# Performance work log

Hardware: AMD Instinct MI355X
Metric: run time of the kernel (lower is better)

The kernel has to match this reference:

```python
import jax, jax.numpy as jnp
import numpy as np

NUM_RBF = 16
TOP_K = 30
NUM_POS_EMB = 16
EDGE_FEATURES = 128
MAX_REL_POS = 32  # ProteinMPNN max_relative_feature


def _rbf(D):
    # D: [...,]; returns [..., NUM_RBF]
    D_min, D_max = 2.0, 22.0
    D_mu = jnp.linspace(D_min, D_max, NUM_RBF)
    D_sigma = (D_max - D_min) / NUM_RBF
    return jnp.exp(-((D[..., None] - D_mu) / D_sigma) ** 2)


def _dist(Xca, mask, eps=1e-6):
    # Xca: [B,L,3], mask: [B,L]
    mask_2D = mask[:, :, None] * mask[:, None, :]  # [B,L,L]
    dX = Xca[:, :, None, :] - Xca[:, None, :, :]
    D = mask_2D * jnp.sqrt(jnp.sum(dX * dX, -1) + eps)
    D_max = jnp.max(D, -1, keepdims=True)
    D_adjust = D + (1.0 - mask_2D) * D_max
    L = Xca.shape[1]
    k = min(TOP_K, L)
    neg_topk, E_idx = jax.lax.top_k(-D_adjust, k)  # smallest distances
    return -neg_topk, E_idx  # D_neighbors:[B,L,K], E_idx:[B,L,K] int32


def _gather_nodes_pair(A, E_idx):
    # A: [B,L], E_idx: [B,L,K] -> [B,L,K]
    return jnp.take_along_axis(A[:, None, :].repeat(A.shape[1], 1), E_idx, axis=2)


def _rbf_pair(A, B_, E_idx):
    # A,B_: [B,L,3]; distances from A[i] to B_[j] for j in neighbors of i
    Bn = jnp.take_along_axis(B_[:, None, :, :].repeat(B_.shape[1], 1), E_idx[..., None].repeat(3, -1), axis=2)  # [B,L,K,3]
    D = jnp.sqrt(jnp.sum((A[:, :, None, :] - Bn) ** 2, -1) + 1e-6)
    return _rbf(D)


def setup_inputs() -> dict:
    key = jax.random.key(0)
    k1, k2, k3, k4 = jax.random.split(key, 4)
    B, L = 8, 2048
    X = jax.random.normal(k1, (B, L, 4, 3), dtype=jnp.float32) * 5.0
    mask = jnp.ones((B, L), dtype=jnp.float32)
    residue_idx = jnp.broadcast_to(jnp.arange(L, dtype=jnp.int32), (B, L))
    chain_labels = jnp.zeros((B, L), dtype=jnp.int32)
    in_dim = NUM_POS_EMB + NUM_RBF * 25  # 16 + 400 = 416
    W_e = jax.random.normal(k2, (in_dim, EDGE_FEATURES), dtype=jnp.float32) * (1.0 / np.sqrt(in_dim))
    b_e = jnp.zeros((EDGE_FEATURES,), dtype=jnp.float32)
    g_e = jnp.ones((EDGE_FEATURES,), dtype=jnp.float32)  # layernorm gamma
    be_ln = jnp.zeros((EDGE_FEATURES,), dtype=jnp.float32)  # layernorm beta
    pe_dim = 2 * MAX_REL_POS + 2  # 66
    W_pe = jax.random.normal(k3, (pe_dim, NUM_POS_EMB), dtype=jnp.float32) * (1.0 / np.sqrt(pe_dim))
    b_pe = jnp.zeros((NUM_POS_EMB,), dtype=jnp.float32)
    return {"X": X, "mask": mask, "residue_idx": residue_idx, "chain_labels": chain_labels,
            "W_e": W_e, "b_e": b_e, "g_e": g_e, "be_ln": be_ln, "W_pe": W_pe, "b_pe": b_pe}


def reference(X, mask, residue_idx, chain_labels, W_e, b_e, g_e, be_ln, W_pe, b_pe):
    # atoms
    N = X[:, :, 0, :]
    Ca = X[:, :, 1, :]
    C = X[:, :, 2, :]
    O = X[:, :, 3, :]
    # virtual Cb (ProteinMPNN formula)
    b = Ca - N
    c = C - Ca
    a = jnp.cross(b, c)
    Cb = -0.58273431 * a + 0.56802827 * b - 0.54067466 * c + Ca

    D_neighbors, E_idx = _dist(Ca, mask)

    atoms = {"N": N, "Ca": Ca, "C": C, "O": O, "Cb": Cb}
    order = ["Ca", "N", "C", "O", "Cb"]
    rbf_list = []
    for ai in order:
        for aj in order:
            if ai == "Ca" and aj == "Ca":
                rbf_list.append(_rbf(D_neighbors))
            else:
                rbf_list.append(_rbf_pair(atoms[ai], atoms[aj], E_idx))
    RBF_all = jnp.concatenate(rbf_list, axis=-1)  # [B,L,K,400]

    # positional encodings (ProteinMPNN style)
    offset = residue_idx[:, :, None] - residue_idx[:, None, :]  # [B,L,L]
    offset = jnp.take_along_axis(offset, E_idx, axis=2)  # [B,L,K]
    d_chains = (chain_labels[:, :, None] == chain_labels[:, None, :]).astype(jnp.int32)
    E_chains = jnp.take_along_axis(d_chains, E_idx, axis=2)  # [B,L,K]
    d = jnp.clip(offset + MAX_REL_POS, 0, 2 * MAX_REL_POS) * E_chains + (1 - E_chains) * (2 * MAX_REL_POS + 1)
    d_onehot = jax.nn.one_hot(d, 2 * MAX_REL_POS + 2, dtype=RBF_all.dtype)
    E_pos = d_onehot @ W_pe + b_pe  # [B,L,K,16]

    E = jnp.concatenate([E_pos, RBF_all], axis=-1)  # [B,L,K,416]
    E = E @ W_e + b_e  # [B,L,K,128]
    # layer norm
    mu = jnp.mean(E, -1, keepdims=True)
    var = jnp.var(E, -1, keepdims=True)
    E = (E - mu) / jnp.sqrt(var + 1e-5) * g_e + be_ln
    return E, E_idx
```

## Files before the change

kernel.cpp:

```cpp
#include <hip/hip_runtime.h>
#include <hip/hip_bf16.h>
#include <stdint.h>

#define BB   8
#define LL   2048
#define KK   30
#define COUT 128
#define FIN  416
#define PE_DIM 16
#define MAXREL 32
#define KSTEPS 13

typedef __attribute__((ext_vector_type(8))) short short8;
typedef __attribute__((ext_vector_type(4))) float f32x4;

__device__ __forceinline__ unsigned int f2bf(float x) {
    unsigned int u = __float_as_uint(x);
    return (u + 0x7fffu + ((u >> 16) & 1u)) >> 16;
}

__device__ __forceinline__ unsigned int packbf2(float a, float b) {
    float2 f; f.x = a; f.y = b;
    __hip_bfloat162 h = __float22bfloat162_rn(f);
    unsigned int u;
    __builtin_memcpy(&u, &h, 4);
    return u;
}

__device__ __forceinline__ short8 as_s8(uint4 u) {
    union { uint4 u; short8 s; } x; x.u = u; return x.s;
}

__device__ __forceinline__ int lanes_below(unsigned long long m) {
    return __builtin_amdgcn_mbcnt_hi((unsigned)(m >> 32),
           __builtin_amdgcn_mbcnt_lo((unsigned)m, 0));
}

__global__ __launch_bounds__(256)
void atoms_kernel(const float* __restrict__ X, float4* __restrict__ atoms4) {
    int idx = blockIdx.x * 256 + threadIdx.x;
    if (idx >= BB * LL) return;
    int b = idx >> 11;
    int i = idx & (LL - 1);
    const float4* xp = reinterpret_cast<const float4*>(X + (size_t)idx * 12);
    float4 p0 = xp[0], p1 = xp[1], p2 = xp[2];
    float Nx = p0.x, Ny = p0.y, Nz = p0.z;
    float Ax = p0.w, Ay = p1.x, Az = p1.y;
    float Cx = p1.z, Cy = p1.w, Cz = p2.x;
    float Ox = p2.y, Oy = p2.z, Oz = p2.w;
    float bx = Ax - Nx, by = Ay - Ny, bz = Az - Nz;
    float cx = Cx - Ax, cy = Cy - Ay, cz = Cz - Az;
    float ax = by * cz - bz * cy;
    float ay = bz * cx - bx * cz;
    float az = bx * cy - by * cx;
    float Cbx = -0.58273431f * ax + 0.56802827f * bx - 0.54067466f * cx + Ax;
    float Cby = -0.58273431f * ay + 0.56802827f * by - 0.54067466f * cy + Ay;
    float Cbz = -0.58273431f * az + 0.56802827f * bz - 0.54067466f * cz + Az;
    float4* ab = atoms4 + (size_t)b * 5 * LL;
    ab[0 * LL + i] = make_float4(Ax, Ay, Az, 0.f);
    ab[1 * LL + i] = make_float4(Nx, Ny, Nz, 0.f);
    ab[2 * LL + i] = make_float4(Cx, Cy, Cz, 0.f);
    ab[3 * LL + i] = make_float4(Ox, Oy, Oz, 0.f);
    ab[4 * LL + i] = make_float4(Cbx, Cby, Cbz, 0.f);
}

__global__ __launch_bounds__(256)
void wfrag_kernel(const float* __restrict__ W_e, unsigned short* __restrict__ wf) {
    int idx = blockIdx.x * 256 + threadIdx.x;
    if (idx >= KSTEPS * 8 * 64) return;
    int lane = idx & 63;
    int tile = idx >> 6;
    int ks = tile >> 3, nt = tile & 7;
    int n  = nt * 16 + (lane & 15);
    int kb = ks * 32 + (lane >> 4) * 8;
    unsigned int p[8];
    #pragma unroll
    for (int j = 0; j < 8; j++) p[j] = f2bf(W_e[(size_t)(kb + j) * COUT + n]);
    uint4 w;
    w.x = p[0] | (p[1] << 16);
    w.y = p[2] | (p[3] << 16);
    w.z = p[4] | (p[5] << 16);
    w.w = p[6] | (p[7] << 16);
    reinterpret_cast<uint4*>(wf)[idx] = w;
}

__global__ __launch_bounds__(256)
void topk_kernel(const float4* __restrict__ atoms4, unsigned short* __restrict__ eidx,
                 float* __restrict__ out_eidx_f) {
    __shared__ unsigned long long skeys[4][32];
    int t = threadIdx.x;
    int wv = t >> 6, ln = t & 63;
    int row = blockIdx.x * 4 + wv;
    int b = row >> 11, i = row & (LL - 1);
    const float4* cab = atoms4 + (size_t)b * 5 * LL;
    float4 pi = cab[i];
    float xi = pi.x, yi = pi.y, zi = pi.z;
    unsigned int bits[32];
    unsigned int mn = 0xffffffffu, lmx = 0u;
    #pragma unroll
    for (int r = 0; r < 32; r++) {
        int j = ln + 64 * r;
        float4 pj = cab[j];
        float dx = __fsub_rn(xi, pj.x);
        float dy = __fsub_rn(yi, pj.y);
        float dz = __fsub_rn(zi, pj.z);
        float s = __fadd_rn(__fadd_rn(__fmul_rn(dx, dx), __fmul_rn(dy, dy)),
                            __fmul_rn(dz, dz));
        s = __fadd_rn(s, 1e-6f);
        float D = __fsqrt_rn(s);
        unsigned int ub = __float_as_uint(D);
        bits[r] = ub;
        mn  = mn  < ub ? mn  : ub;
        lmx = lmx > ub ? lmx : ub;
    }
    #pragma unroll
    for (int off = 1; off < 64; off <<= 1) {
        unsigned int om = __shfl_xor(mn, off);
        unsigned int ox = __shfl_xor(lmx, off);
        mn  = mn  < om ? mn  : om;
        lmx = lmx < ox ? lmx : ox;
    }
    unsigned int lo = __builtin_amdgcn_readfirstlane(mn);
    unsigned int hi = __builtin_amdgcn_readfirstlane(lmx);

    while (lo < hi) {
        unsigned int mid = lo + ((hi - lo) >> 1);
        int c = 0;
        #pragma unroll
        for (int r = 0; r < 32; r++)
            c += __popcll(__ballot(bits[r] <= mid));
        if (c >= KK) hi = mid; else lo = mid + 1;
    }
    unsigned int T = lo;

    int clt = 0;
    #pragma unroll
    for (int r = 0; r < 32; r++)
        clt += __popcll(__ballot(bits[r] < T));
    int need_ties = KK - clt;

    int base = 0, tiebase = 0;
    #pragma unroll
    for (int r = 0; r < 32; r++) {
        bool lt = bits[r] < T;
        bool eq = bits[r] == T;
        unsigned long long bq = __ballot(eq);
        int trk = tiebase + lanes_below(bq);
        bool sel = lt || (eq && trk < need_ties);
        unsigned long long bs = __ballot(sel);
        int pos = base + lanes_below(bs);
        if (sel)
            skeys[wv][pos] = ((unsigned long long)bits[r] << 11) |
                             (unsigned long long)(unsigned)(ln + 64 * r);
        base    += __popcll(bs);
        tiebase += __popcll(bq);
    }
    asm volatile("s_waitcnt lgkmcnt(0)" ::: "memory");

    unsigned long long mykey = (ln < KK) ? skeys[wv][ln] : ~0ull;
    int rank = 0;
    for (int s = 0; s < KK; s++) {
        unsigned long long other = __shfl(mykey, s);
        rank += (other < mykey) ? 1 : 0;
    }
    if (ln < KK) {
        int jw = (int)(mykey & 2047ull);
        eidx[(size_t)row * KK + rank] = (unsigned short)jw;
        out_eidx_f[(size_t)row * KK + rank] = (float)jw;
    }
}

__global__ __launch_bounds__(256)
void edge_kernel(const float4* __restrict__ atoms4, const unsigned short* __restrict__ eidx,
                 const int* __restrict__ residx, const int* __restrict__ chains,
                 const float* __restrict__ W_pe, const float* __restrict__ b_pe,
                 const unsigned short* __restrict__ wfrag,
                 const float* __restrict__ b_e,  const float* __restrict__ g_e,
                 const float* __restrict__ be_ln, float* __restrict__ outE) {
    __shared__ float d25L[4][16][26];
    int t = threadIdx.x;
    int w = t >> 6, l = t & 63;
    int m16 = l & 15, quad = l >> 4;
    int ebase = blockIdx.x * 64;
    int b0 = ebase / (LL * KK);
    int e0 = ebase + w * 16;

    int eL  = e0 + m16;
    int biL = eL / KK;
    int i2L = biL & (LL - 1);
    int jv  = eidx[eL];
    int offv  = residx[biL] - residx[(b0 << 11) + jv];
    int samev = (chains[biL] == chains[(b0 << 11) + jv]);
    int dd = offv + MAXREL;
    dd = dd < 0 ? 0 : (dd > 2 * MAXREL ? 2 * MAXREL : dd);
    int dsl = samev ? dd : (2 * MAXREL + 1);

    const float4* ap = atoms4 + (size_t)b0 * 5 * LL;

    #pragma unroll
    for (int rr = 0; rr < 7; rr++) {
        int task = rr * 64 + l;
        if (task < 400) {
            int p  = task >> 4, el = task & 15;
            int ai = (p * 205) >> 10;
            int aj = p - ai * 5;
            int i2 = __shfl(i2L, el);
            int j2 = __shfl(jv,  el);
            float4 A  = ap[(size_t)ai * LL + i2];
            float4 Bv = ap[(size_t)aj * LL + j2];
            float dx = A.x - Bv.x, dy = A.y - Bv.y, dz = A.z - Bv.z;
            d25L[w][el][p] = __builtin_amdgcn_sqrtf(dx * dx + dy * dy + dz * dz + 1e-6f);
        }
    }
    asm volatile("s_waitcnt lgkmcnt(0)" ::: "memory");

    const float QQ = 0.10273981f;

    f32x4 acc[8];
    #pragma unroll
    for (int nt = 0; nt < 8; nt++) acc[nt] = (f32x4){0.f, 0.f, 0.f, 0.f};

    const uint4* Bg = reinterpret_cast<const uint4*>(wfrag);
    #pragma unroll
    for (int ks = 0; ks < KSTEPS; ks++) {
        int k8 = ks * 4 + quad;
        float v[8];
        if (k8 < 2) {
            const float4* wp4 = reinterpret_cast<const float4*>(W_pe + dsl * PE_DIM + k8 * 8);
            const float4* bp4 = reinterpret_cast<const float4*>(b_pe + k8 * 8);
            float4 wa = wp4[0], wb = wp4[1];
            float4 ba = bp4[0], bb = bp4[1];
            v[0] = wa.x + ba.x; v[1] = wa.y + ba.y; v[2] = wa.z + ba.z; v[3] = wa.w + ba.w;
            v[4] = wb.x + bb.x; v[5] = wb.y + bb.y; v[6] = wb.z + bb.z; v[7] = wb.w + bb.w;
        } else {
            int p = (k8 - 2) >> 1;
            float d = d25L[w][m16][p];
            float mu_a = (k8 & 1) ? 18.0f : 7.3333333f;
            float t4 = fminf(d - mu_a, 50.0f);
            float e4 = __builtin_amdgcn_exp2f(-0.92332483f * (t4 * t4));
            float g  = __builtin_amdgcn_exp2f(__builtin_fmaf(2.4621995f, t4, -1.6414664f));
            float u  = QQ * __builtin_amdgcn_rcpf(g);
            v[4] = e4;
            float e = e4, r = g;
            e *= r; v[5] = e; r *= QQ; e *= r; v[6] = e; r *= QQ; e *= r; v[7] = e;
            e = e4; r = u;
            e *= r; v[3] = e; r *= QQ; e *= r; v[2] = e; r *= QQ; e *= r; v[1] = e;
            r *= QQ; e *= r; v[0] = e;
        }
        uint4 pk;
        pk.x = packbf2(v[0], v[1]);
        pk.y = packbf2(v[2], v[3]);
        pk.z = packbf2(v[4], v[5]);
        pk.w = packbf2(v[6], v[7]);
        short8 afrag = as_s8(pk);
        #pragma unroll
        for (int nt = 0; nt < 8; nt++) {
            uint4 bu = Bg[((size_t)(ks * 8 + nt)) * 64 + l];
            acc[nt] = __builtin_amdgcn_mfma_f32_16x16x32_bf16(afrag, as_s8(bu), acc[nt], 0, 0, 0);
        }
    }

    float be_[8], ge_[8], bl_[8];
    #pragma unroll
    for (int nt = 0; nt < 8; nt++) {
        be_[nt] = b_e[nt * 16 + m16];
        ge_[nt] = g_e[nt * 16 + m16];
        bl_[nt] = be_ln[nt * 16 + m16];
    }

    #pragma unroll
    for (int r = 0; r < 4; r++) {
        float vv[8];
        float s = 0.f, s2 = 0.f;
        #pragma unroll
        for (int nt = 0; nt < 8; nt++) {
            float x = acc[nt][r] + be_[nt];
            vv[nt] = x;
            s += x; s2 += x * x;
        }
        #pragma unroll
        for (int off = 1; off < 16; off <<= 1) {
            s  += __shfl_xor(s,  off);
            s2 += __shfl_xor(s2, off);
        }
        float mu  = s * (1.0f / 128.0f);
        float var = s2 * (1.0f / 128.0f) - mu * mu;
        float rs  = rsqrtf(var + 1e-5f);
        int e = e0 + quad * 4 + r;
        float* op = outE + (size_t)e * COUT + m16;
        #pragma unroll
        for (int nt = 0; nt < 8; nt++)
            op[nt * 16] = (vv[nt] - mu) * rs * ge_[nt] + bl_[nt];
    }
}

extern "C" void kernel_launch(void* const* d_in, const int* in_sizes, int n_in,
                              void* d_out, int out_size, void* d_ws, size_t ws_size,
                              hipStream_t stream) {
    const float* X      = (const float*)d_in[0];
    const int*   residx = (const int*)d_in[2];
    const int*   chains = (const int*)d_in[3];
    const float* W_e    = (const float*)d_in[4];
    const float* b_e    = (const float*)d_in[5];
    const float* g_e    = (const float*)d_in[6];
    const float* be_ln  = (const float*)d_in[7];
    const float* W_pe   = (const float*)d_in[8];
    const float* b_pe   = (const float*)d_in[9];

    float* outE     = (float*)d_out;
    float* outEidxF = outE + (size_t)BB * LL * KK * COUT;

    float4*         atoms4 = (float4*)d_ws;
    unsigned short* eidx   = (unsigned short*)(atoms4 + (size_t)BB * 5 * LL);
    unsigned short* wf     = eidx + (size_t)BB * LL * KK;

    atoms_kernel<<<(BB * LL + 255) / 256, 256, 0, stream>>>(X, atoms4);
    wfrag_kernel<<<(KSTEPS * 8 * 64 + 255) / 256, 256, 0, stream>>>(W_e, wf);
    topk_kernel <<<BB * LL / 4, 256, 0, stream>>>(atoms4, eidx, outEidxF);
    edge_kernel <<<(BB * LL * KK) / 64, 256, 0, stream>>>(
        atoms4, eidx, residx, chains, W_pe, b_pe, wf, b_e, g_e, be_ln, outE);
}
```

Measured before the change: 447.8 us.

## Switch edge GEMM to 32x32x16 MFMA with 32 edges per wave

Replaces the 16x16x32 bf16 MFMA tiling in the edge kernel with 32x32x16 MFMA. Each wave now processes 32 edges and each block 128, and the weight fragments are re-laid out for the new operand shape. Each lane computes one distance-pair RBF chunk per k-step, so the per-k-step branching is simpler and fewer B fragment loads are needed per edge. The accumulator grows to 64 floats per lane, which raises register pressure, and the layer norm now needs a 32-lane shuffle reduction.

```diff
diff --git a/kernel.cpp b/kernel.cpp
--- a/kernel.cpp
+++ b/kernel.cpp
@@ -9,10 +9,12 @@
 #define FIN  416
 #define PE_DIM 16
 #define MAXREL 32
-#define KSTEPS 13
-
-typedef __attribute__((ext_vector_type(8))) short short8;
-typedef __attribute__((ext_vector_type(4))) float f32x4;
+#define KSTEPS 26
+#define WTILES (KSTEPS * 4)
+
+typedef __attribute__((ext_vector_type(8)))  short short8;
+typedef __attribute__((ext_vector_type(4)))  float f32x4;
+typedef __attribute__((ext_vector_type(16))) float f32x16;
 
 __device__ __forceinline__ unsigned int f2bf(float x) {
     unsigned int u = __float_as_uint(x);
@@ -67,12 +69,12 @@
 __global__ __launch_bounds__(256)
 void wfrag_kernel(const float* __restrict__ W_e, unsigned short* __restrict__ wf) {
     int idx = blockIdx.x * 256 + threadIdx.x;
-    if (idx >= KSTEPS * 8 * 64) return;
+    if (idx >= WTILES * 64) return;
     int lane = idx & 63;
     int tile = idx >> 6;
-    int ks = tile >> 3, nt = tile & 7;
-    int n  = nt * 16 + (lane & 15);
-    int kb = ks * 32 + (lane >> 4) * 8;
+    int ks = tile >> 2, nt = tile & 3;
+    int n  = nt * 32 + (lane & 31);
+    int kb = ks * 16 + (lane >> 5) * 8;
     unsigned int p[8];
     #pragma unroll
     for (int j = 0; j < 8; j++) p[j] = f2bf(W_e[(size_t)(kb + j) * COUT + n]);
@@ -177,15 +179,15 @@
                  const unsigned short* __restrict__ wfrag,
                  const float* __restrict__ b_e,  const float* __restrict__ g_e,
                  const float* __restrict__ be_ln, float* __restrict__ outE) {
-    __shared__ float d25L[4][16][26];
+    __shared__ float d25L[4][32][26];
     int t = threadIdx.x;
     int w = t >> 6, l = t & 63;
-    int m16 = l & 15, quad = l >> 4;
-    int ebase = blockIdx.x * 64;
+    int e32 = l & 31, half = l >> 5;
+    int ebase = blockIdx.x * 128;
     int b0 = ebase / (LL * KK);
-    int e0 = ebase + w * 16;
-
-    int eL  = e0 + m16;
+    int e0 = ebase + w * 32;
+
+    int eL  = e0 + e32;
     int biL = eL / KK;
     int i2L = biL & (LL - 1);
     int jv  = eidx[eL];
@@ -198,10 +200,10 @@
     const float4* ap = atoms4 + (size_t)b0 * 5 * LL;
 
     #pragma unroll
-    for (int rr = 0; rr < 7; rr++) {
+    for (int rr = 0; rr < 13; rr++) {
         int task = rr * 64 + l;
-        if (task < 400) {
-            int p  = task >> 4, el = task & 15;
+        if (task < 800) {
+            int p  = task >> 5, el = task & 31;
             int ai = (p * 205) >> 10;
             int aj = p - ai * 5;
             int i2 = __shfl(i2L, el);
@@ -215,27 +217,32 @@
     asm volatile("s_waitcnt lgkmcnt(0)" ::: "memory");
 
     const float QQ = 0.10273981f;
-
-    f32x4 acc[8];
-    #pragma unroll
-    for (int nt = 0; nt < 8; nt++) acc[nt] = (f32x4){0.f, 0.f, 0.f, 0.f};
+    float mu_a = half ? 18.0f : 7.3333333f;
+
+    f32x16 acc[4];
+    #pragma unroll
+    for (int nt = 0; nt < 4; nt++)
+        #pragma unroll
+        for (int r = 0; r < 16; r++) acc[nt][r] = 0.f;
 
     const uint4* Bg = reinterpret_cast<const uint4*>(wfrag);
     #pragma unroll
     for (int ks = 0; ks < KSTEPS; ks++) {
-        int k8 = ks * 4 + quad;
+        uint4 bu0 = Bg[((size_t)(ks * 4 + 0)) * 64 + l];
+        uint4 bu1 = Bg[((size_t)(ks * 4 + 1)) * 64 + l];
+        uint4 bu2 = Bg[((size_t)(ks * 4 + 2)) * 64 + l];
+        uint4 bu3 = Bg[((size_t)(ks * 4 + 3)) * 64 + l];
+
         float v[8];
-        if (k8 < 2) {
-            const float4* wp4 = reinterpret_cast<const float4*>(W_pe + dsl * PE_DIM + k8 * 8);
-            const float4* bp4 = reinterpret_cast<const float4*>(b_pe + k8 * 8);
+        if (ks == 0) {
+            const float4* wp4 = reinterpret_cast<const float4*>(W_pe + dsl * PE_DIM + half * 8);
+            const float4* bp4 = reinterpret_cast<const float4*>(b_pe + half * 8);
             float4 wa = wp4[0], wb = wp4[1];
             float4 ba = bp4[0], bb = bp4[1];
             v[0] = wa.x + ba.x; v[1] = wa.y + ba.y; v[2] = wa.z + ba.z; v[3] = wa.w + ba.w;
             v[4] = wb.x + bb.x; v[5] = wb.y + bb.y; v[6] = wb.z + bb.z; v[7] = wb.w + bb.w;
         } else {
-            int p = (k8 - 2) >> 1;
-            float d = d25L[w][m16][p];
-            float mu_a = (k8 & 1) ? 18.0f : 7.3333333f;
+            float d = d25L[w][e32][ks - 1];
             float t4 = fminf(d - mu_a, 50.0f);
             float e4 = __builtin_amdgcn_exp2f(-0.92332483f * (t4 * t4));
             float g  = __builtin_amdgcn_exp2f(__builtin_fmaf(2.4621995f, t4, -1.6414664f));
@@ -253,44 +260,43 @@
         pk.z = packbf2(v[4], v[5]);
         pk.w = packbf2(v[6], v[7]);
         short8 afrag = as_s8(pk);
-        #pragma unroll
-        for (int nt = 0; nt < 8; nt++) {
-            uint4 bu = Bg[((size_t)(ks * 8 + nt)) * 64 + l];
-            acc[nt] = __builtin_amdgcn_mfma_f32_16x16x32_bf16(afrag, as_s8(bu), acc[nt], 0, 0, 0);
-        }
-    }
-
-    float be_[8], ge_[8], bl_[8];
-    #pragma unroll
-    for (int nt = 0; nt < 8; nt++) {
-        be_[nt] = b_e[nt * 16 + m16];
-        ge_[nt] = g_e[nt * 16 + m16];
-        bl_[nt] = be_ln[nt * 16 + m16];
-    }
-
-    #pragma unroll
-    for (int r = 0; r < 4; r++) {
-        float vv[8];
+        acc[0] = __builtin_amdgcn_mfma_f32_32x32x16_bf16(afrag, as_s8(bu0), acc[0], 0, 0, 0);
+        acc[1] = __builtin_amdgcn_mfma_f32_32x32x16_bf16(afrag, as_s8(bu1), acc[1], 0, 0, 0);
+        acc[2] = __builtin_amdgcn_mfma_f32_32x32x16_bf16(afrag, as_s8(bu2), acc[2], 0, 0, 0);
+        acc[3] = __builtin_amdgcn_mfma_f32_32x32x16_bf16(afrag, as_s8(bu3), acc[3], 0, 0, 0);
+    }
+
+    float be_[4], ge_[4], bl_[4];
+    #pragma unroll
+    for (int nt = 0; nt < 4; nt++) {
+        be_[nt] = b_e[nt * 32 + e32];
+        ge_[nt] = g_e[nt * 32 + e32];
+        bl_[nt] = be_ln[nt * 32 + e32];
+    }
+
+    #pragma unroll
+    for (int reg = 0; reg < 16; reg++) {
+        float vv[4];
         float s = 0.f, s2 = 0.f;
         #pragma unroll
-        for (int nt = 0; nt < 8; nt++) {
-            float x = acc[nt][r] + be_[nt];
+        for (int nt = 0; nt < 4; nt++) {
+            float x = acc[nt][reg] + be_[nt];
             vv[nt] = x;
             s += x; s2 += x * x;
         }
         #pragma unroll
-        for (int off = 1; off < 16; off <<= 1) {
+        for (int off = 1; off < 32; off <<= 1) {
             s  += __shfl_xor(s,  off);
             s2 += __shfl_xor(s2, off);
         }
         float mu  = s * (1.0f / 128.0f);
         float var = s2 * (1.0f / 128.0f) - mu * mu;
         float rs  = rsqrtf(var + 1e-5f);
-        int e = e0 + quad * 4 + r;
-        float* op = outE + (size_t)e * COUT + m16;
-        #pragma unroll
-        for (int nt = 0; nt < 8; nt++)
-            op[nt * 16] = (vv[nt] - mu) * rs * ge_[nt] + bl_[nt];
+        int e = e0 + (reg & 3) + 8 * (reg >> 2) + 4 * half;
+        float* op = outE + (size_t)e * COUT + e32;
+        #pragma unroll
+        for (int nt = 0; nt < 4; nt++)
+            op[nt * 32] = (vv[nt] - mu) * rs * ge_[nt] + bl_[nt];
     }
 }
 
@@ -315,8 +321,8 @@
     unsigned short* wf     = eidx + (size_t)BB * LL * KK;
 
     atoms_kernel<<<(BB * LL + 255) / 256, 256, 0, stream>>>(X, atoms4);
-    wfrag_kernel<<<(KSTEPS * 8 * 64 + 255) / 256, 256, 0, stream>>>(W_e, wf);
+    wfrag_kernel<<<(WTILES * 64 + 255) / 256, 256, 0, stream>>>(W_e, wf);
     topk_kernel <<<BB * LL / 4, 256, 0, stream>>>(atoms4, eidx, outEidxF);
-    edge_kernel <<<(BB * LL * KK) / 64, 256, 0, stream>>>(
+    edge_kernel <<<(BB * LL * KK) / 128, 256, 0, stream>>>(
         atoms4, eidx, residx, chains, W_pe, b_pe, wf, b_e, g_e, be_ln, outE);
 }
```

After: 436.7 us. 1.03x faster.
